# Optimization experiments

Measured on AMD Instinct MI355X. Metric: run time of the kernel, lower is better.

Reference implementation:

```python
import jax, jax.numpy as jnp
import numpy as np

H_DIM = 64
GRID = 8
NS = 2.0  # neighborhood_size
S = 256   # number of sequences (scenes)
P = 64    # pedestrians per sequence
EPS = 1e-5


def setup_inputs() -> dict:
    key = jax.random.key(0)
    k = jax.random.split(key, 6)
    N = S * P
    G = GRID * GRID
    h_states = jax.random.normal(k[0], (1, N, H_DIM), jnp.float32)
    end_pos = jax.random.normal(k[1], (N, 2), jnp.float32)
    starts = (jnp.arange(S, dtype=jnp.int32) * P)
    seq_start_end = jnp.stack([starts, starts + P], axis=1)  # (S, 2)
    # mlp_pool: Linear(G*H_DIM -> H_DIM) + BatchNorm1d + ReLU
    W = jax.random.normal(k[2], (G * H_DIM, H_DIM), jnp.float32) / np.sqrt(G * H_DIM)
    b = jnp.zeros((H_DIM,), jnp.float32)
    gamma = jnp.ones((H_DIM,), jnp.float32)
    beta = jnp.zeros((H_DIM,), jnp.float32)
    return {"h_states": h_states, "seq_start_end": seq_start_end, "end_pos": end_pos,
            "W": W, "b": b, "gamma": gamma, "beta": beta}


def reference(h_states, seq_start_end, end_pos, W, b, gamma, beta):
    nseq = seq_start_end.shape[0]          # S (static)
    N = end_pos.shape[0]
    Hd = h_states.shape[-1]
    nped = N // nseq                       # P (static; equal-length sequences)
    G = GRID * GRID
    half = NS / 2.0

    h = h_states.reshape(N, Hd).reshape(nseq, nped, Hd)     # (S, P, H)
    pos = end_pos.reshape(nseq, nped, 2)                    # (S, P, 2)

    # bounds per center pedestrian i
    tl_x = pos[..., 0] - half   # (S, P)
    tl_y = pos[..., 1] + half
    br_x = pos[..., 0] + half
    br_y = pos[..., 1] - half

    # pairwise: axis 1 = center i, axis 2 = other k
    ox = pos[:, None, :, 0]     # (S, 1, P)
    oy = pos[:, None, :, 1]
    cell_x = jnp.floor((ox - tl_x[:, :, None]) / NS * GRID)
    cell_y = jnp.floor((tl_y[:, :, None] - oy) / NS * GRID)
    grid = cell_x + cell_y * GRID                            # (S, P, P)

    oob = ((ox >= br_x[:, :, None]) | (ox <= tl_x[:, :, None]) |
           (oy >= tl_y[:, :, None]) | (oy <= br_y[:, :, None]))
    diag = jnp.eye(nped, dtype=bool)[None]                   # self excluded (within_bound[0::P+1]=1)
    valid = (~oob) & (~diag)

    grid_i = jnp.clip(grid.astype(jnp.int32), 0, G - 1)      # masked entries don't matter
    seq_off = (jnp.arange(nseq, dtype=jnp.int32)[:, None, None] * nped
               + jnp.arange(nped, dtype=jnp.int32)[None, :, None]) * G
    dummy = nseq * nped * G
    ids = jnp.where(valid, seq_off + grid_i, dummy)          # (S, P, P)

    # data for (s, i, k) is hidden of other k (curr_hidden.repeat(num_ped, 1))
    data = jnp.broadcast_to(h[:, None, :, :], (nseq, nped, nped, Hd)).reshape(-1, Hd)
    pooled = jax.ops.segment_sum(data, ids.reshape(-1), num_segments=dummy + 1)[:-1]
    x = pooled.reshape(N, G * Hd)                            # (N, G*H), row i = concat over grid cells

    # mlp_pool: Linear -> BatchNorm1d (train mode, biased var) -> ReLU
    x = x @ W + b
    mu = jnp.mean(x, axis=0)
    var = jnp.mean((x - mu) ** 2, axis=0)
    x = gamma * (x - mu) / jnp.sqrt(var + EPS) + beta
    return jnp.maximum(x, 0.0)
```

## Files before the change

kernel.cpp:

```cpp
#include <hip/hip_runtime.h>
#include <hip/hip_bf16.h>


#define NSEQ 256
#define NTOT (NSEQ*64)
#define EPSV 1e-5f

typedef __attribute__((ext_vector_type(8))) short short8;
typedef __attribute__((ext_vector_type(4))) float f32x4;
typedef unsigned short ushort_t;

__device__ __forceinline__ ushort_t f2b(float f) {
    __hip_bfloat16 h = __float2bfloat16(f);
    return *reinterpret_cast<ushort_t*>(&h);
}
__device__ __forceinline__ int kperm(int k) {
    return ((k >> 5)*2 + ((k & 7) >> 2))*16 + ((k >> 3) & 3)*4 + (k & 3);
}

__global__ __launch_bounds__(256) void sp_transpose(
    const float* __restrict__ W, short* __restrict__ Wt, float* __restrict__ statbuf)
{
    __shared__ __align__(16) float Tl[64*68];
    const int b = blockIdx.x, tid = threadIdx.x;
    if (b == 0) {
        #pragma unroll
        for (int q = 0; q < 8; ++q) statbuf[q*256 + tid] = 0.0f;
    }
    const float* wg = W + (size_t)b*4096;
    for (int m = 0; m < 4; ++m) {
        int c = m*256 + tid;
        int k = c >> 4, t0 = (c & 15)*4;
        *(f32x4*)(Tl + k*68 + t0) = *(const f32x4*)(wg + k*64 + t0);
    }
    __syncthreads();
    for (int m = 0; m < 2; ++m) {
        int q = m*256 + tid;
        int col = q >> 3, k0 = (q & 7)*8;
        short8 o;
        #pragma unroll
        for (int i2 = 0; i2 < 8; ++i2)
            o[i2] = (short)f2b(Tl[kperm(k0 + i2)*68 + col]);
        *(short8*)(Wt + ((size_t)(b*64 + col)*64 + k0)) = o;
    }
}

#define SM_CM   9216
#define SM_POS  11264
#define SM_HF   11776
#define SM_XS1  8704
#define SM_RED  17408
#define SM_TOT  19968

__global__ __launch_bounds__(512, 4) void sp_main(
    const float* __restrict__ h, const float* __restrict__ pos,
    const short* __restrict__ Wt, const float* __restrict__ bvec,
    float* __restrict__ X, float* __restrict__ statbuf)
{
    __shared__ __align__(16) char smem[SM_TOT];
    ushort_t*      Ht = (ushort_t*)(smem);
    unsigned char* cm = (unsigned char*)(smem + SM_CM);
    float*         px = (float*)(smem + SM_POS);
    float*         py = px + 64;
    short*         Hf = (short*)(smem + SM_HF);

    const int b    = blockIdx.x;
    const int seq  = b >> 1;
    const int row0 = (b & 1) * 32;
    const int base = seq * 64;
    const int tid  = threadIdx.x;
    const int lane = tid & 63, w = tid >> 6;
    const int ln15 = lane & 15, ln4 = lane >> 4;
    const int xph  = (b >> 3) & 7;

    if (tid < 64) { px[tid] = pos[(base + tid)*2]; py[tid] = pos[(base + tid)*2 + 1]; }
    for (int m = 0; m < 2; ++m) {
        int c = m*512 + tid;
        int j = c >> 4, t0 = (c & 15)*4;
        f32x4 v = *(const f32x4*)(h + (size_t)(base + j)*64 + t0);
        #pragma unroll
        for (int u = 0; u < 4; ++u) Ht[(t0 + u)*72 + j] = f2b(v[u]);
    }
    __syncthreads();

    for (int m = 0; m < 4; ++m) {
        int p = m*512 + tid;
        int il = p >> 6, j = p & 63;
        int i  = row0 + il;
        unsigned char val = 255;
        if (i != j) {
            float ax = px[i], ay = py[i], ox = px[j], oy = py[j];
            float tlx = ax - 1.0f, tly = ay + 1.0f, brx = ax + 1.0f, bry = ay - 1.0f;
            bool oob = (ox >= brx) | (ox <= tlx) | (oy >= tly) | (oy <= bry);
            if (!oob) {
                int g = (int)(floorf((ox - tlx)*4.0f) + floorf((tly - oy)*4.0f)*8.0f);
                g = g < 0 ? 0 : (g > 63 ? 63 : g);
                val = (unsigned char)g;
            }
        }
        cm[il*64 + j] = val;
    }
    if (tid < 64) {
        #pragma unroll
        for (int f = 0; f < 8; ++f) {
            int mt = f >> 1, kt2 = f & 1;
            short8 v = *(const short8*)(Ht + (mt*16 + ln15)*72 + kt2*32 + ln4*8);
            *(short8*)(Hf + (f*64 + lane)*8) = v;
        }
    }
    __syncthreads();

    unsigned ohw[2][2][2];
    {
        const unsigned w8 = (unsigned)(w * 8);
        #pragma unroll
        for (int rt = 0; rt < 2; ++rt)
            #pragma unroll
            for (int kt = 0; kt < 2; ++kt) {
                const unsigned* cp = (const unsigned*)(cm + (rt*16 + ln15)*64 + kt*32 + ln4*8);
                #pragma unroll
                for (int half = 0; half < 2; ++half) {
                    unsigned cw = cp[half], oh = 0u;
                    #pragma unroll
                    for (int u = 0; u < 4; ++u) {
                        unsigned d = ((cw >> (8*u)) & 255u) - w8;
                        if (d < 8u) oh |= (1u << d) << (8*u);
                    }
                    ohw[rt][kt][half] = oh;
                }
            }
    }

    f32x4 acc[2][4];
    #pragma unroll
    for (int rt = 0; rt < 2; ++rt)
        #pragma unroll
        for (int nt = 0; nt < 4; ++nt) acc[rt][nt] = (f32x4){0.f,0.f,0.f,0.f};

    for (int cc = 0; cc < 8; ++cc) {
        const int c2 = (cc + xph) & 7;
        const int g  = w*8 + c2;
        const short* wgp = Wt + (size_t)g*4096;
        short8 bw[2][4];
        #pragma unroll
        for (int kt = 0; kt < 2; ++kt)
            #pragma unroll
            for (int nt = 0; nt < 4; ++nt)
                bw[kt][nt] = *(const short8*)(wgp + (nt*16 + ln15)*64 + kt*32 + ln4*8);

        #pragma unroll
        for (int rt = 0; rt < 2; ++rt) {
            short8 sf[2];
            #pragma unroll
            for (int kt = 0; kt < 2; ++kt) {
                unsigned t0 = (ohw[rt][kt][0] >> c2) & 0x01010101u;
                unsigned t1 = (ohw[rt][kt][1] >> c2) & 0x01010101u;
                union { unsigned u[4]; short8 s; } sfu;
                sfu.u[0] = ((t0 & 1u)          | ((t0 << 8) & 0x10000u)) * 0x3F80u;
                sfu.u[1] = (((t0 >> 16) & 1u)  | ((t0 >> 8) & 0x10000u)) * 0x3F80u;
                sfu.u[2] = ((t1 & 1u)          | ((t1 << 8) & 0x10000u)) * 0x3F80u;
                sfu.u[3] = (((t1 >> 16) & 1u)  | ((t1 >> 8) & 0x10000u)) * 0x3F80u;
                sf[kt] = sfu.s;
            }
            f32x4 pt[4];
            #pragma unroll
            for (int mt = 0; mt < 4; ++mt) pt[mt] = (f32x4){0.f,0.f,0.f,0.f};
            #pragma unroll
            for (int kt2 = 0; kt2 < 2; ++kt2) {
                short8 hm[4];
                #pragma unroll
                for (int mt = 0; mt < 4; ++mt)
                    hm[mt] = *(const short8*)(Hf + (((mt*2 + kt2)*64 + lane))*8);
                #pragma unroll
                for (int mt = 0; mt < 4; ++mt)
                    pt[mt] = __builtin_amdgcn_mfma_f32_16x16x32_bf16(hm[mt], sf[kt2], pt[mt], 0, 0, 0);
            }
            #pragma unroll
            for (int kt = 0; kt < 2; ++kt) {
                short8 af;
                #pragma unroll
                for (int r = 0; r < 4; ++r) {
                    af[r]     = (short)f2b(pt[2*kt    ][r]);
                    af[4 + r] = (short)f2b(pt[2*kt + 1][r]);
                }
                #pragma unroll
                for (int nt = 0; nt < 4; ++nt)
                    acc[rt][nt] = __builtin_amdgcn_mfma_f32_16x16x32_bf16(af, bw[kt][nt], acc[rt][nt], 0, 0, 0);
            }
        }
    }
    __syncthreads();

    float* Xs0 = (float*)smem;
    float* Xs1 = (float*)(smem + SM_XS1);
    for (int step = 0; step < 4; ++step) {
        if ((w & 3) == step) {
            float* Xs = (w < 4) ? Xs0 : Xs1;
            #pragma unroll
            for (int rt = 0; rt < 2; ++rt)
                #pragma unroll
                for (int nt = 0; nt < 4; ++nt)
                    #pragma unroll
                    for (int r = 0; r < 4; ++r) {
                        int row = rt*16 + ln4*4 + r;
                        int col = nt*16 + ln15;
                        if (step == 0) Xs[row*68 + col]  = acc[rt][nt][r];
                        else           Xs[row*68 + col] += acc[rt][nt][r];
                    }
        }
        __syncthreads();
    }

    {
        const int lr = tid >> 4, c0 = (tid & 15)*4;
        float* xg = X + (size_t)(base + row0 + lr)*64 + c0;
        f32x4 v;
        #pragma unroll
        for (int u = 0; u < 4; ++u) {
            int o = lr*68 + c0 + u;
            v[u] = Xs0[o] + Xs1[o] + bvec[c0 + u];
        }
        *(f32x4*)xg = v;
    }

    {
        float* red1 = (float*)(smem + SM_RED);
        float* red2 = red1 + 256;
        if (tid < 256) {
            int col = tid & 63, rg = tid >> 6;
            float bc = bvec[col], s1 = 0.f, s2 = 0.f;
            for (int ii = 0; ii < 8; ++ii) {
                int o = (rg*8 + ii)*68 + col;
                float xv = Xs0[o] + Xs1[o] + bc;
                s1 += xv; s2 += xv*xv;
            }
            red1[rg*64 + col] = s1;
            red2[rg*64 + col] = s2;
        }
        __syncthreads();
        if (tid < 128) {
            int hs = tid >> 6, c2 = tid & 63;
            const float* r0 = hs ? red2 : red1;
            float v = r0[c2] + r0[64 + c2] + r0[128 + c2] + r0[192 + c2];
            atomicAdd(statbuf + (b & 15)*128 + tid, v);
        }
    }
}

__global__ __launch_bounds__(256) void sp_finish(
    float* __restrict__ X, const float* __restrict__ statbuf,
    const float* __restrict__ gamma, const float* __restrict__ beta)
{
    __shared__ float scale[64], shift[64];
    const int b = blockIdx.x, tid = threadIdx.x;

    if (tid < 64) {
        const float inv_n = 1.0f / (float)NTOT;
        float s1 = 0.f, s2 = 0.f;
        #pragma unroll
        for (int s = 0; s < 16; ++s) {
            s1 += statbuf[s*128 + tid];
            s2 += statbuf[s*128 + 64 + tid];
        }
        float mu  = s1 * inv_n;
        float var = s2 * inv_n - mu*mu;
        float sc  = gamma[tid] / sqrtf(var + EPSV);
        scale[tid] = sc;
        shift[tid] = beta[tid] - mu*sc;
    }
    __syncthreads();
    #pragma unroll
    for (int q = 0; q < 4; ++q) {
        size_t idx4 = (size_t)b*1024 + q*256 + tid;
        f32x4 v = ((f32x4*)X)[idx4];
        int c0 = ((int)idx4*4) & 63;
        #pragma unroll
        for (int u = 0; u < 4; ++u)
            v[u] = fmaxf(v[u]*scale[c0 + u] + shift[c0 + u], 0.0f);
        ((f32x4*)X)[idx4] = v;
    }
}

extern "C" void kernel_launch(void* const* d_in, const int* in_sizes, int n_in,
                              void* d_out, int out_size, void* d_ws, size_t ws_size,
                              hipStream_t stream)
{
    const float* h     = (const float*)d_in[0];
    const float* pos   = (const float*)d_in[2];
    const float* W     = (const float*)d_in[3];
    const float* bvec  = (const float*)d_in[4];
    const float* gamma = (const float*)d_in[5];
    const float* beta  = (const float*)d_in[6];

    float* X       = (float*)d_out;
    short* Wt      = (short*)d_ws;
    float* statbuf = (float*)((char*)d_ws + 524288);

    sp_transpose<<<64,      256, 0, stream>>>(W, Wt, statbuf);
    sp_main     <<<NSEQ*2,  512, 0, stream>>>(h, pos, Wt, bvec, X, statbuf);
    sp_finish   <<<NSEQ,    256, 0, stream>>>(X, statbuf, gamma, beta);
}
```

Measured before the change: 111.2 us.

## Process a whole sequence per 1024-thread block instead of half per block

Merges the two half-sequence blocks into one 1024-thread block per sequence. The 64x64 cell map, the hidden-state transpose and the position loads are then computed once per sequence instead of being duplicated across two blocks. The grid halves to 256 blocks and LDS per block roughly doubles. This lowers redundant setup work, but 1024-thread blocks with launch_bounds(1024,4) constrain registers and give fewer, larger blocks for the scheduler on 256 CUs.

After: 111.2 us. Within noise of the previous version (+0.0%).

```diff
diff --git a/kernel.cpp b/kernel.cpp
--- a/kernel.cpp
+++ b/kernel.cpp
@@ -45,14 +45,17 @@
     }
 }
 
-#define SM_CM   9216
-#define SM_POS  11264
-#define SM_HF   11776
-#define SM_XS1  8704
-#define SM_RED  17408
-#define SM_TOT  19968
-
-__global__ __launch_bounds__(512, 4) void sp_main(
+#define SM_CM    9216
+#define SM_POS   13312
+#define SM_HF    13824
+#define SM_XSA1  8704
+#define SM_XSB0  17408
+#define SM_XSB1  26112
+#define SM_REDA  34816
+#define SM_REDB  36864
+#define SM_TOT   38912
+
+__global__ __launch_bounds__(1024, 4) void sp_main(
     const float* __restrict__ h, const float* __restrict__ pos,
     const short* __restrict__ Wt, const float* __restrict__ bvec,
     float* __restrict__ X, float* __restrict__ statbuf)
@@ -65,18 +68,18 @@
     short*         Hf = (short*)(smem + SM_HF);
 
     const int b    = blockIdx.x;
-    const int seq  = b >> 1;
-    const int row0 = (b & 1) * 32;
-    const int base = seq * 64;
+    const int base = b * 64;
     const int tid  = threadIdx.x;
     const int lane = tid & 63, w = tid >> 6;
+    const int wl   = w & 7;
+    const int half = w >> 3;
+    const int row0 = half * 32;
     const int ln15 = lane & 15, ln4 = lane >> 4;
     const int xph  = (b >> 3) & 7;
 
     if (tid < 64) { px[tid] = pos[(base + tid)*2]; py[tid] = pos[(base + tid)*2 + 1]; }
-    for (int m = 0; m < 2; ++m) {
-        int c = m*512 + tid;
-        int j = c >> 4, t0 = (c & 15)*4;
+    {
+        int j = tid >> 4, t0 = (tid & 15)*4;
         f32x4 v = *(const f32x4*)(h + (size_t)(base + j)*64 + t0);
         #pragma unroll
         for (int u = 0; u < 4; ++u) Ht[(t0 + u)*72 + j] = f2b(v[u]);
@@ -84,9 +87,8 @@
     __syncthreads();
 
     for (int m = 0; m < 4; ++m) {
-        int p = m*512 + tid;
-        int il = p >> 6, j = p & 63;
-        int i  = row0 + il;
+        int p = m*1024 + tid;
+        int i = p >> 6, j = p & 63;
         unsigned char val = 255;
         if (i != j) {
             float ax = px[i], ay = py[i], ox = px[j], oy = py[j];
@@ -98,7 +100,7 @@
                 val = (unsigned char)g;
             }
         }
-        cm[il*64 + j] = val;
+        cm[i*64 + j] = val;
     }
     if (tid < 64) {
         #pragma unroll
@@ -112,21 +114,21 @@
 
     unsigned ohw[2][2][2];
     {
-        const unsigned w8 = (unsigned)(w * 8);
+        const unsigned w8 = (unsigned)(wl * 8);
         #pragma unroll
         for (int rt = 0; rt < 2; ++rt)
             #pragma unroll
             for (int kt = 0; kt < 2; ++kt) {
-                const unsigned* cp = (const unsigned*)(cm + (rt*16 + ln15)*64 + kt*32 + ln4*8);
-                #pragma unroll
-                for (int half = 0; half < 2; ++half) {
-                    unsigned cw = cp[half], oh = 0u;
+                const unsigned* cp = (const unsigned*)(cm + (row0 + rt*16 + ln15)*64 + kt*32 + ln4*8);
+                #pragma unroll
+                for (int hf2 = 0; hf2 < 2; ++hf2) {
+                    unsigned cw = cp[hf2], oh = 0u;
                     #pragma unroll
                     for (int u = 0; u < 4; ++u) {
                         unsigned d = ((cw >> (8*u)) & 255u) - w8;
                         if (d < 8u) oh |= (1u << d) << (8*u);
                     }
-                    ohw[rt][kt][half] = oh;
+                    ohw[rt][kt][hf2] = oh;
                 }
             }
     }
@@ -139,7 +141,7 @@
 
     for (int cc = 0; cc < 8; ++cc) {
         const int c2 = (cc + xph) & 7;
-        const int g  = w*8 + c2;
+        const int g  = wl*8 + c2;
         const short* wgp = Wt + (size_t)g*4096;
         short8 bw[2][4];
         #pragma unroll
@@ -191,11 +193,14 @@
     }
     __syncthreads();
 
-    float* Xs0 = (float*)smem;
-    float* Xs1 = (float*)(smem + SM_XS1);
+    float* XsA0 = (float*)smem;
+    float* XsA1 = (float*)(smem + SM_XSA1);
+    float* XsB0 = (float*)(smem + SM_XSB0);
+    float* XsB1 = (float*)(smem + SM_XSB1);
     for (int step = 0; step < 4; ++step) {
-        if ((w & 3) == step) {
-            float* Xs = (w < 4) ? Xs0 : Xs1;
+        if ((wl & 3) == step) {
+            float* Xs = half ? ((wl < 4) ? XsB0 : XsB1)
+                             : ((wl < 4) ? XsA0 : XsA1);
             #pragma unroll
             for (int rt = 0; rt < 2; ++rt)
                 #pragma unroll
@@ -212,37 +217,48 @@
     }
 
     {
-        const int lr = tid >> 4, c0 = (tid & 15)*4;
-        float* xg = X + (size_t)(base + row0 + lr)*64 + c0;
+        const int hh = tid >> 9, t = tid & 511;
+        const int lr = t >> 4, c0 = (t & 15)*4;
+        const float* Y0 = hh ? XsB0 : XsA0;
+        const float* Y1 = hh ? XsB1 : XsA1;
+        float* xg = X + (size_t)(base + hh*32 + lr)*64 + c0;
         f32x4 v;
         #pragma unroll
         for (int u = 0; u < 4; ++u) {
             int o = lr*68 + c0 + u;
-            v[u] = Xs0[o] + Xs1[o] + bvec[c0 + u];
+            v[u] = Y0[o] + Y1[o] + bvec[c0 + u];
         }
         *(f32x4*)xg = v;
     }
 
     {
-        float* red1 = (float*)(smem + SM_RED);
-        float* red2 = red1 + 256;
-        if (tid < 256) {
-            int col = tid & 63, rg = tid >> 6;
+        float* redA1 = (float*)(smem + SM_REDA);
+        float* redA2 = redA1 + 256;
+        float* redB1 = (float*)(smem + SM_REDB);
+        float* redB2 = redB1 + 256;
+        if (tid < 256 || (tid >= 512 && tid < 768)) {
+            int hh = tid >> 9, t = tid & 255;
+            int col = t & 63, rg = t >> 6;
+            const float* Y0 = hh ? XsB0 : XsA0;
+            const float* Y1 = hh ? XsB1 : XsA1;
+            float* r1 = hh ? redB1 : redA1;
+            float* r2 = hh ? redB2 : redA2;
             float bc = bvec[col], s1 = 0.f, s2 = 0.f;
             for (int ii = 0; ii < 8; ++ii) {
                 int o = (rg*8 + ii)*68 + col;
-                float xv = Xs0[o] + Xs1[o] + bc;
+                float xv = Y0[o] + Y1[o] + bc;
                 s1 += xv; s2 += xv*xv;
             }
-            red1[rg*64 + col] = s1;
-            red2[rg*64 + col] = s2;
+            r1[rg*64 + col] = s1;
+            r2[rg*64 + col] = s2;
         }
         __syncthreads();
-        if (tid < 128) {
-            int hs = tid >> 6, c2 = tid & 63;
-            const float* r0 = hs ? red2 : red1;
+        if (tid < 128 || (tid >= 512 && tid < 640)) {
+            int hh = tid >> 9, t = tid & 127;
+            int hs = t >> 6, c2 = t & 63;
+            const float* r0 = hh ? (hs ? redB2 : redB1) : (hs ? redA2 : redA1);
             float v = r0[c2] + r0[64 + c2] + r0[128 + c2] + r0[192 + c2];
-            atomicAdd(statbuf + (b & 15)*128 + tid, v);
+            atomicAdd(statbuf + (b & 15)*128 + hs*64 + c2, v);
         }
     }
 }
@@ -296,7 +312,7 @@
     short* Wt      = (short*)d_ws;
     float* statbuf = (float*)((char*)d_ws + 524288);
 
-    sp_transpose<<<64,      256, 0, stream>>>(W, Wt, statbuf);
-    sp_main     <<<NSEQ*2,  512, 0, stream>>>(h, pos, Wt, bvec, X, statbuf);
-    sp_finish   <<<NSEQ,    256, 0, stream>>>(X, statbuf, gamma, beta);
-}
+    sp_transpose<<<64,   256,  0, stream>>>(W, Wt, statbuf);
+    sp_main     <<<NSEQ, 1024, 0, stream>>>(h, pos, Wt, bvec, X, statbuf);
+    sp_finish   <<<NSEQ, 256,  0, stream>>>(X, statbuf, gamma, beta);
+}
```
